# Optimization experiments

Hardware: AMD Instinct MI355X
Metric: run time of the kernel (lower is better)

The kernel has to match this reference:

```python
import jax, jax.numpy as jnp
import numpy as np

N, E, IN, H, C, L = 40000, 640000, 256, 128, 64, 4
ALPHA, LAMB = 0.5, 1.0


def setup_inputs() -> dict:
    key = jax.random.key(0)
    ks = jax.random.split(key, 8)
    x = jax.random.normal(ks[0], (N, IN), jnp.float32)
    src = jax.random.randint(ks[1], (E,), 0, N, jnp.int32)
    dst = jax.random.randint(ks[2], (E,), 0, N, jnp.int32)
    s_in = 1.0 / np.sqrt(IN)
    s_h = 1.0 / np.sqrt(H)
    fc1_w = jax.random.normal(ks[3], (IN, H), jnp.float32) * s_in
    fc1_b = jnp.zeros((H,), jnp.float32)
    W1 = jax.random.normal(ks[4], (L, H, H), jnp.float32) * s_h   # GCN2Conv weight1 per layer
    W2 = jax.random.normal(ks[5], (L, H, H), jnp.float32) * s_h   # GCN2Conv weight2 (initial-residual proj)
    bgc = jnp.zeros((L, H), jnp.float32)                          # GCN2Conv bias per layer
    fc2_w = jax.random.normal(ks[6], (H, C), jnp.float32) * s_h
    fc2_b = jnp.zeros((C,), jnp.float32)
    return dict(x=x, fc1_w=fc1_w, fc1_b=fc1_b, W1=W1, W2=W2, bgc=bgc,
                fc2_w=fc2_w, fc2_b=fc2_b, src=src, dst=dst)


def reference(x, fc1_w, fc1_b, W1, W2, bgc, fc2_w, fc2_b, src, dst):
    ones = jnp.ones((E,), x.dtype)
    # symmetric 'both' normalization: deg_out^{-1/2} on src side, deg_in^{-1/2} on dst side
    deg_out = jnp.clip(jax.ops.segment_sum(ones, src, num_segments=N), 1.0)
    deg_in = jnp.clip(jax.ops.segment_sum(ones, dst, num_segments=N), 1.0)
    norm_s = (deg_out ** -0.5)[:, None]
    norm_d = (deg_in ** -0.5)[:, None]

    # feature_preprocess: dropout (eval = identity) -> fc1 -> relu
    h0 = jax.nn.relu(x @ fc1_w + fc1_b)          # [N, H]
    h = h0
    for l in range(L):
        beta = float(np.log(LAMB / (l + 1) + 1.0))
        identity = h
        # sparse neighbor aggregation (SpMM via gather + segment_sum)
        agg = jax.ops.segment_sum((h * norm_s)[src], dst, num_segments=N) * norm_d
        feat = (1.0 - ALPHA) * agg               # smoothed features
        f0 = ALPHA * h0                          # initial residual
        rst = (1.0 - beta) * (feat + f0) + beta * (feat @ W1[l] + f0 @ W2[l]) + bgc[l]
        h = jax.nn.relu(rst + identity)          # outer residual + activation (dropout eval = identity)
    return h @ fc2_w + fc2_b                     # [N, C]
```

## Files before the change

### kernel.cpp

```cpp
#include <hip/hip_runtime.h>
#include <math.h>

#define N_NODES 40000
#define N_EDGES 640000
#define IN_F 256
#define H_F 128
#define C_F 64
#define L_LAYERS 4
#define SCAN_BLKS 157
#define N_CHUNKS 64
#define CHUNK_E 10000
#define HIST_WORDS 10000

typedef short short8 __attribute__((ext_vector_type(8)));
typedef unsigned short ushort8 __attribute__((ext_vector_type(8)));
typedef float f32x4 __attribute__((ext_vector_type(4)));

__device__ inline short to_bf16(float f) {
    unsigned u = __builtin_bit_cast(unsigned, f);
    unsigned r = (u + 0x7FFFu + ((u >> 16) & 1u)) >> 16;
    return (short)r;
}
__device__ inline float bf16_to_f(unsigned short u) {
    unsigned v = ((unsigned)u) << 16;
    return __builtin_bit_cast(float, v);
}

__device__ inline int block_excl_scan(int v, int* wsum, int* tot) {
    int tid = threadIdx.x;
    int lane = tid & 63, wid = tid >> 6;
    int incl = v;
    #pragma unroll
    for (int off = 1; off < 64; off <<= 1) {
        int t = __shfl_up(incl, off, 64);
        if (lane >= off) incl += t;
    }
    if (lane == 63) wsum[wid] = incl;
    __syncthreads();
    int prefix = 0, total = 0;
    #pragma unroll
    for (int w = 0; w < 4; w++) {
        int s = wsum[w];
        if (w < wid) prefix += s;
        total += s;
    }
    *tot = total;
    return prefix + incl - v;
}

#define CVT8(dstv, p) {                                                         \
    float4 _v0 = *(const float4*)(p); float4 _v1 = *(const float4*)((p) + 4);   \
    dstv[0] = to_bf16(_v0.x); dstv[1] = to_bf16(_v0.y);                         \
    dstv[2] = to_bf16(_v0.z); dstv[3] = to_bf16(_v0.w);                         \
    dstv[4] = to_bf16(_v1.x); dstv[5] = to_bf16(_v1.y);                         \
    dstv[6] = to_bf16(_v1.z); dstv[7] = to_bf16(_v1.w); }

__global__ __launch_bounds__(256) void prep_hist(const int* __restrict__ src,
                                                 const int* __restrict__ dst,
                                                 int* __restrict__ chunk_dst,
                                                 int* __restrict__ chunk_src,
                                                 unsigned char* __restrict__ lrank8,
                                                 const float* __restrict__ fc1_w,
                                                 const float* __restrict__ W1,
                                                 const float* __restrict__ W2,
                                                 const float* __restrict__ fc2_w,
                                                 float s0, float s1, float s2, float s3,
                                                 short* __restrict__ fc1_wT,
                                                 short* __restrict__ WcatT,
                                                 short* __restrict__ fc2_wT) {
    __shared__ int cntp[HIST_WORDS];
    int blk = blockIdx.x;
    if (blk < 128) {
        int role_dst = (blk < 64);
        int w = role_dst ? blk : blk - 64;
        const int* idx = role_dst ? dst : src;
        int base = w * CHUNK_E;
        for (int i = threadIdx.x; i < HIST_WORDS; i += 256) cntp[i] = 0;
        __syncthreads();
        if (role_dst) {
            for (int i = threadIdx.x; i < CHUNK_E; i += 256) {
                int d = idx[base + i];
                int sh = (d & 3) * 8;
                int old = atomicAdd(&cntp[d >> 2], 1 << sh);
                lrank8[base + i] = (unsigned char)((old >> sh) & 0xff);
            }
        } else {
            for (int i = threadIdx.x; i < CHUNK_E; i += 256) {
                int s = idx[base + i];
                atomicAdd(&cntp[s >> 2], 1 << ((s & 3) * 8));
            }
        }
        __syncthreads();
        int* outp = role_dst ? (chunk_dst + w * HIST_WORDS) : (chunk_src + w * HIST_WORDS);
        for (int i = threadIdx.x; i < HIST_WORDS; i += 256) outp[i] = cntp[i];
        return;
    }
    int i = (blk - 128) * 256 + threadIdx.x;
    if (i < 128 * 256) {
        int n = i >> 8, k = i & 255;
        fc1_wT[i] = to_bf16(fc1_w[k * H_F + n]);
    }
    if (i < 4 * 128 * 256) {
        int l = i >> 15; int r = i & 32767; int n = r >> 8; int k = r & 255;
        float sc = (l == 0) ? s0 : (l == 1) ? s1 : (l == 2) ? s2 : s3;
        float w = (k < 128) ? W1[l * 16384 + k * H_F + n]
                            : W2[l * 16384 + (k - 128) * H_F + n];
        WcatT[i] = to_bf16(sc * w);
    }
    if (i < 64 * 128) {
        int n = i >> 7, k = i & 127;
        fc2_wT[i] = to_bf16(fc2_w[k * C_F + n]);
    }
}

__global__ __launch_bounds__(256) void fc1_scan(const float* __restrict__ x,
                                                const short* __restrict__ wT,
                                                const float* __restrict__ b,
                                                unsigned short* __restrict__ h0b,
                                                const int* __restrict__ chunk_dst,
                                                const int* __restrict__ chunk_src,
                                                int* __restrict__ base32,
                                                float* __restrict__ rsq_in,
                                                float* __restrict__ rsq_out,
                                                float* __restrict__ sq_out,
                                                int* __restrict__ row_local,
                                                int* __restrict__ blk_sum) {
    __shared__ int wsum[4];
    int blk = blockIdx.x;
    if (blk >= 1250) {
        int sb = blk - 1250;
        int n = sb * 256 + threadIdx.x;
        int deg = 0, word = 0, sh = 0;
        if (n < N_NODES) {
            word = n >> 2; sh = (n & 3) * 8;
            #pragma unroll 4
            for (int w = 0; w < N_CHUNKS; w++)
                deg += (chunk_dst[w * HIST_WORDS + word] >> sh) & 0xff;
        }
        int tot;
        int excl = block_excl_scan(deg, wsum, &tot);
        if (n < N_NODES) {
            row_local[n] = excl;
            int run = excl;
            #pragma unroll 4
            for (int w = 0; w < N_CHUNKS; w++) {
                int v = (chunk_dst[w * HIST_WORDS + word] >> sh) & 0xff;
                base32[(size_t)w * N_NODES + n] = run;
                run += v;
            }
            int so = 0;
            #pragma unroll 4
            for (int w = 0; w < N_CHUNKS; w++)
                so += (chunk_src[w * HIST_WORDS + word] >> sh) & 0xff;
            float fd = (float)(deg < 1 ? 1 : deg);
            float fs = (float)(so < 1 ? 1 : so);
            rsq_in[n] = 1.0f / sqrtf(fd);
            rsq_out[n] = 1.0f / sqrtf(fs);
            sq_out[n] = sqrtf(fs);
        }
        if (threadIdx.x == 0) blk_sum[sb] = tot;
        return;
    }
    int tid = threadIdx.x;
    int wave = tid >> 6, lane = tid & 63;
    int rowgrp = wave >> 1, chalf = wave & 1;
    int m = lane & 15, quad = lane >> 4;
    int row = blk * 32 + rowgrp * 16 + m;
    const float* xr = x + (size_t)row * IN_F + quad * 8;
    short8 afrag[8];
    #pragma unroll
    for (int ks = 0; ks < 8; ks++) {
        CVT8(afrag[ks], xr + ks * 32);
    }
    #pragma unroll
    for (int ci = 0; ci < 4; ci += 2) {
        int c = chalf * 4 + ci;
        f32x4 acc0 = {0.f, 0.f, 0.f, 0.f};
        f32x4 acc1 = {0.f, 0.f, 0.f, 0.f};
        const short* b0p = wT + (size_t)(c * 16 + m) * IN_F + quad * 8;
        const short* b1p = b0p + 16 * IN_F;
        #pragma unroll
        for (int ks = 0; ks < 8; ks++) {
            short8 b0 = *(const short8*)(b0p + ks * 32);
            short8 b1 = *(const short8*)(b1p + ks * 32);
            acc0 = __builtin_amdgcn_mfma_f32_16x16x32_bf16(afrag[ks], b0, acc0, 0, 0, 0);
            acc1 = __builtin_amdgcn_mfma_f32_16x16x32_bf16(afrag[ks], b1, acc1, 0, 0, 0);
        }
        int col0 = c * 16 + m;
        int rbase = blk * 32 + rowgrp * 16 + quad * 4;
        float bg0 = b[col0], bg1 = b[col0 + 16];
        #pragma unroll
        for (int r = 0; r < 4; r++) {
            size_t idx2 = (size_t)(rbase + r) * H_F + col0;
            float v0 = acc0[r] + bg0;
            float v1 = acc1[r] + bg1;
            v0 = v0 > 0.f ? v0 : 0.f;
            v1 = v1 > 0.f ? v1 : 0.f;
            h0b[idx2] = (unsigned short)to_bf16(v0);
            h0b[idx2 + 16] = (unsigned short)to_bf16(v1);
        }
    }
}

__global__ __launch_bounds__(256) void fill_fused(const int* __restrict__ src,
                                                  const int* __restrict__ dst,
                                                  const unsigned char* __restrict__ lrank8,
                                                  const int* __restrict__ base32,
                                                  const int* __restrict__ row_local,
                                                  const int* __restrict__ blk_sum,
                                                  unsigned short* __restrict__ col16,
                                                  int* __restrict__ row_ptr,
                                                  const unsigned short* __restrict__ h0b,
                                                  const float* __restrict__ rsq_out,
                                                  unsigned short* __restrict__ h0s) {
    __shared__ int wsum[4];
    __shared__ int blk_offL[SCAN_BLKS];
    int tid = threadIdx.x;
    {
        int v = (tid < SCAN_BLKS) ? blk_sum[tid] : 0;
        int tot;
        int excl = block_excl_scan(v, wsum, &tot);
        if (tid < SCAN_BLKS) blk_offL[tid] = excl;
    }
    __syncthreads();

    int blk = blockIdx.x;
    if (blk < 2500) {
        int e = blk * 256 + tid;
        int w = e / CHUNK_E;
        int s = src[e], d = dst[e];
        int rp = blk_offL[d >> 8] + base32[(size_t)w * N_NODES + d] + (int)lrank8[e];
        col16[rp] = (unsigned short)s;
        return;
    }
    if (blk < 2657) {
        int n = (blk - 2500) * 256 + tid;
        if (n < N_NODES) row_ptr[n] = blk_offL[n >> 8] + row_local[n];
        if (blk == 2500 && tid == 0) row_ptr[N_NODES] = N_EDGES;
        return;
    }
    int j = (blk - 2657) * 2048 + tid * 8;
    ushort8 u = *(const ushort8*)(h0b + j);
    float rs = rsq_out[j >> 7];
    ushort8 o;
    #pragma unroll
    for (int jj = 0; jj < 8; jj++) o[jj] = (unsigned short)to_bf16(rs * bf16_to_f(u[jj]));
    *(ushort8*)(h0s + j) = o;
}

__global__ __launch_bounds__(256) void spmm_kernel(const unsigned short* __restrict__ hs,
                                                   const int* __restrict__ row_ptr,
                                                   const unsigned short* __restrict__ col16,
                                                   const float* __restrict__ rsq_in,
                                                   unsigned short* __restrict__ aggb) {
    int wave = threadIdx.x >> 6, lane = threadIdx.x & 63;
    int slot = lane >> 4, fi = lane & 15;
    int n = blockIdx.x * 4 + wave;
    int e0 = row_ptr[n], e1 = row_ptr[n + 1];
    float a[8] = {};
    for (int e = e0 + slot; e < e1; e += 16) {
        int eb = e + 4, ec = e + 8, ed = e + 12;
        int c0 = col16[e];
        int c1 = (eb < e1) ? col16[eb] : c0;  float w1 = (eb < e1) ? 1.f : 0.f;
        int c2 = (ec < e1) ? col16[ec] : c0;  float w2 = (ec < e1) ? 1.f : 0.f;
        int c3 = (ed < e1) ? col16[ed] : c0;  float w3 = (ed < e1) ? 1.f : 0.f;
        ushort8 u0 = *(const ushort8*)(hs + (size_t)c0 * H_F + fi * 8);
        ushort8 u1 = *(const ushort8*)(hs + (size_t)c1 * H_F + fi * 8);
        ushort8 u2 = *(const ushort8*)(hs + (size_t)c2 * H_F + fi * 8);
        ushort8 u3 = *(const ushort8*)(hs + (size_t)c3 * H_F + fi * 8);
        #pragma unroll
        for (int j = 0; j < 8; j++) {
            a[j] += bf16_to_f(u0[j]) + w1 * bf16_to_f(u1[j])
                  + w2 * bf16_to_f(u2[j]) + w3 * bf16_to_f(u3[j]);
        }
    }
    #pragma unroll
    for (int mask = 16; mask <= 32; mask <<= 1) {
        #pragma unroll
        for (int j = 0; j < 8; j++) a[j] += __shfl_xor(a[j], mask, 64);
    }
    if (slot == 0) {
        float rs = rsq_in[n];
        ushort8 r;
        #pragma unroll
        for (int j = 0; j < 8; j++) r[j] = (unsigned short)to_bf16(rs * a[j]);
        *(ushort8*)(aggb + (size_t)n * H_F + fi * 8) = r;
    }
}

__global__ __launch_bounds__(256) void combine_mfma(const unsigned short* __restrict__ aggb,
                                                    const unsigned short* __restrict__ h0b,
                                                    const unsigned short* __restrict__ hs_in,
                                                    const short* __restrict__ wT,
                                                    const float* __restrict__ bgc,
                                                    const float* __restrict__ rsq_out,
                                                    const float* __restrict__ sq_out,
                                                    float omb5,
                                                    unsigned short* __restrict__ hs_out) {
    int tid = threadIdx.x;
    int wave = tid >> 6, lane = tid & 63;
    int rowgrp = wave >> 1, chalf = wave & 1;
    int m = lane & 15, quad = lane >> 4;
    int row = blockIdx.x * 32 + rowgrp * 16 + m;
    const unsigned short* aggr = aggb + (size_t)row * H_F + quad * 8;
    const unsigned short* h0r  = h0b + (size_t)row * H_F + quad * 8;
    short8 afrag[8];
    #pragma unroll
    for (int ks = 0; ks < 4; ks++) {
        afrag[ks] = __builtin_bit_cast(short8, *(const ushort8*)(aggr + ks * 32));
        afrag[ks + 4] = __builtin_bit_cast(short8, *(const ushort8*)(h0r + ks * 32));
    }
    #pragma unroll
    for (int ci = 0; ci < 4; ci += 2) {
        int c = chalf * 4 + ci;
        f32x4 acc0 = {0.f, 0.f, 0.f, 0.f};
        f32x4 acc1 = {0.f, 0.f, 0.f, 0.f};
        const short* b0p = wT + (size_t)(c * 16 + m) * 256 + quad * 8;
        const short* b1p = b0p + 16 * 256;
        #pragma unroll
        for (int ks = 0; ks < 8; ks++) {
            short8 b0 = *(const short8*)(b0p + ks * 32);
            short8 b1 = *(const short8*)(b1p + ks * 32);
            acc0 = __builtin_amdgcn_mfma_f32_16x16x32_bf16(afrag[ks], b0, acc0, 0, 0, 0);
            acc1 = __builtin_amdgcn_mfma_f32_16x16x32_bf16(afrag[ks], b1, acc1, 0, 0, 0);
        }
        int col0 = c * 16 + m;
        int rbase = blockIdx.x * 32 + rowgrp * 16 + quad * 4;
        float bg0 = bgc[col0], bg1 = bgc[col0 + 16];
        #pragma unroll
        for (int r = 0; r < 4; r++) {
            int rw = rbase + r;
            size_t idx = (size_t)rw * H_F + col0;
            float sq = sq_out[rw];
            float rsq = rsq_out[rw];
            float s0 = bf16_to_f(aggb[idx]) + bf16_to_f(h0b[idx]);
            float s1 = bf16_to_f(aggb[idx + 16]) + bf16_to_f(h0b[idx + 16]);
            float v0 = omb5 * s0 + acc0[r] + bg0 + sq * bf16_to_f(hs_in[idx]);
            float v1 = omb5 * s1 + acc1[r] + bg1 + sq * bf16_to_f(hs_in[idx + 16]);
            v0 = v0 > 0.f ? v0 : 0.f;
            v1 = v1 > 0.f ? v1 : 0.f;
            hs_out[idx] = (unsigned short)to_bf16(rsq * v0);
            hs_out[idx + 16] = (unsigned short)to_bf16(rsq * v1);
        }
    }
}

__global__ __launch_bounds__(256) void fc2_mfma(const unsigned short* __restrict__ hs,
                                                const float* __restrict__ sq_out,
                                                const short* __restrict__ wT,
                                                const float* __restrict__ b,
                                                float* __restrict__ out) {
    int tid = threadIdx.x;
    int wave = tid >> 6, lane = tid & 63;
    int m = lane & 15, quad = lane >> 4;
    int row = blockIdx.x * 64 + wave * 16 + m;
    const unsigned short* hr = hs + (size_t)row * H_F + quad * 8;
    float sq = sq_out[row];
    short8 afrag[4];
    #pragma unroll
    for (int ks = 0; ks < 4; ks++) {
        ushort8 u = *(const ushort8*)(hr + ks * 32);
        #pragma unroll
        for (int j = 0; j < 8; j++) afrag[ks][j] = to_bf16(sq * bf16_to_f(u[j]));
    }
    #pragma unroll
    for (int c = 0; c < 4; c += 2) {
        f32x4 acc0 = {0.f, 0.f, 0.f, 0.f};
        f32x4 acc1 = {0.f, 0.f, 0.f, 0.f};
        const short* b0p = wT + (size_t)(c * 16 + m) * H_F + quad * 8;
        const short* b1p = b0p + 16 * H_F;
        #pragma unroll
        for (int ks = 0; ks < 4; ks++) {
            short8 b0 = *(const short8*)(b0p + ks * 32);
            short8 b1 = *(const short8*)(b1p + ks * 32);
            acc0 = __builtin_amdgcn_mfma_f32_16x16x32_bf16(afrag[ks], b0, acc0, 0, 0, 0);
            acc1 = __builtin_amdgcn_mfma_f32_16x16x32_bf16(afrag[ks], b1, acc1, 0, 0, 0);
        }
        int col0 = c * 16 + m;
        int rbase = blockIdx.x * 64 + wave * 16 + quad * 4;
        float bg0 = b[col0], bg1 = b[col0 + 16];
        #pragma unroll
        for (int r = 0; r < 4; r++) {
            size_t idx = (size_t)(rbase + r) * C_F + col0;
            out[idx] = acc0[r] + bg0;
            out[idx + 16] = acc1[r] + bg1;
        }
    }
}

extern "C" void kernel_launch(void* const* d_in, const int* in_sizes, int n_in,
                              void* d_out, int out_size, void* d_ws, size_t ws_size,
                              hipStream_t stream) {
    const float* x     = (const float*)d_in[0];
    const float* fc1_w = (const float*)d_in[1];
    const float* fc1_b = (const float*)d_in[2];
    const float* W1    = (const float*)d_in[3];
    const float* W2    = (const float*)d_in[4];
    const float* bgc   = (const float*)d_in[5];
    const float* fc2_w = (const float*)d_in[6];
    const float* fc2_b = (const float*)d_in[7];
    const int*   src   = (const int*)d_in[8];
    const int*   dst   = (const int*)d_in[9];
    float* out = (float*)d_out;

    char* p = (char*)d_ws;
    auto alloc = [&](size_t bytes) {
        char* r = p;
        p += (bytes + 255) & ~(size_t)255;
        return r;
    };
    int*   chunk_dst = (int*)alloc((size_t)N_CHUNKS * HIST_WORDS * 4);
    int*   chunk_src = (int*)alloc((size_t)N_CHUNKS * HIST_WORDS * 4);
    int*   base32    = (int*)alloc((size_t)N_CHUNKS * N_NODES * 4);
    unsigned char* lrank8 = (unsigned char*)alloc((size_t)N_EDGES);
    float* rsq_in  = (float*)alloc((size_t)N_NODES * 4);
    float* rsq_out = (float*)alloc((size_t)N_NODES * 4);
    float* sq_out  = (float*)alloc((size_t)N_NODES * 4);
    int*   row_ptr   = (int*)alloc((size_t)(N_NODES + 1) * 4);
    int*   row_local = (int*)alloc((size_t)N_NODES * 4);
    int*   blk_sum   = (int*)alloc((size_t)SCAN_BLKS * 4);
    unsigned short* col16 = (unsigned short*)alloc((size_t)N_EDGES * 2);
    unsigned short* aggb = (unsigned short*)alloc((size_t)N_NODES * H_F * 2);
    unsigned short* h0b  = (unsigned short*)alloc((size_t)N_NODES * H_F * 2);
    unsigned short* h0s  = (unsigned short*)alloc((size_t)N_NODES * H_F * 2);
    unsigned short* hAs  = (unsigned short*)alloc((size_t)N_NODES * H_F * 2);
    unsigned short* hBs  = (unsigned short*)alloc((size_t)N_NODES * H_F * 2);
    short* fc1_wT  = (short*)alloc((size_t)128 * 256 * 2);
    short* WcatT   = (short*)alloc((size_t)4 * 128 * 256 * 2);
    short* fc2_wT  = (short*)alloc((size_t)64 * 128 * 2);

    float beta[4], wscale[4], omb5[4];
    for (int l = 0; l < 4; l++) {
        beta[l] = (float)log(1.0 / (double)(l + 1) + 1.0);
        wscale[l] = 0.5f * beta[l];
        omb5[l] = 0.5f * (1.f - beta[l]);
    }

    prep_hist<<<640, 256, 0, stream>>>(src, dst, chunk_dst, chunk_src, lrank8,
                                       fc1_w, W1, W2, fc2_w,
                                       wscale[0], wscale[1], wscale[2], wscale[3],
                                       fc1_wT, WcatT, fc2_wT);
    fc1_scan<<<1407, 256, 0, stream>>>(x, fc1_wT, fc1_b, h0b,
                                       chunk_dst, chunk_src, base32,
                                       rsq_in, rsq_out, sq_out, row_local, blk_sum);
    fill_fused<<<5157, 256, 0, stream>>>(src, dst, lrank8, base32, row_local, blk_sum,
                                         col16, row_ptr, h0b, rsq_out, h0s);

    const unsigned short* sp_in[4] = {h0s, hAs, hBs, hAs};
    unsigned short* out_b[4]       = {hAs, hBs, hAs, hBs};
    for (int l = 0; l < L_LAYERS; l++) {
        spmm_kernel<<<N_NODES / 4, 256, 0, stream>>>(sp_in[l], row_ptr, col16,
                                                     rsq_in, aggb);
        combine_mfma<<<N_NODES / 32, 256, 0, stream>>>(aggb, h0b, sp_in[l],
                                                       WcatT + (size_t)l * 128 * 256,
                                                       bgc + (size_t)l * H_F,
                                                       rsq_out, sq_out, omb5[l],
                                                       out_b[l]);
    }
    fc2_mfma<<<N_NODES / 64, 256, 0, stream>>>(hBs, sq_out, fc2_wT, fc2_b, out);
}
```

Measured before the change: 370.7 us.

## Store scaled node features in feature-chunked layout for cache-local SpMM gathers

```diff
diff --git a/kernel.cpp b/kernel.cpp
--- a/kernel.cpp
+++ b/kernel.cpp
@@ -11,6 +11,8 @@
 #define N_CHUNKS 64
 #define CHUNK_E 10000
 #define HIST_WORDS 10000
+#define FCH 4
+#define FCW 32
 
 typedef short short8 __attribute__((ext_vector_type(8)));
 typedef unsigned short ushort8 __attribute__((ext_vector_type(8)));
@@ -127,8 +129,8 @@
                                                 int* __restrict__ blk_sum) {
     __shared__ int wsum[4];
     int blk = blockIdx.x;
-    if (blk >= 1250) {
-        int sb = blk - 1250;
+    if (blk >= 625) {
+        int sb = blk - 625;
         int n = sb * 256 + threadIdx.x;
         int deg = 0, word = 0, sh = 0;
         if (n < N_NODES) {
@@ -163,9 +165,8 @@
     }
     int tid = threadIdx.x;
     int wave = tid >> 6, lane = tid & 63;
-    int rowgrp = wave >> 1, chalf = wave & 1;
     int m = lane & 15, quad = lane >> 4;
-    int row = blk * 32 + rowgrp * 16 + m;
+    int row = blk * 64 + wave * 16 + m;
     const float* xr = x + (size_t)row * IN_F + quad * 8;
     short8 afrag[8];
     #pragma unroll
@@ -173,8 +174,7 @@
         CVT8(afrag[ks], xr + ks * 32);
     }
     #pragma unroll
-    for (int ci = 0; ci < 4; ci += 2) {
-        int c = chalf * 4 + ci;
+    for (int c = 0; c < 8; c += 2) {
         f32x4 acc0 = {0.f, 0.f, 0.f, 0.f};
         f32x4 acc1 = {0.f, 0.f, 0.f, 0.f};
         const short* b0p = wT + (size_t)(c * 16 + m) * IN_F + quad * 8;
@@ -187,7 +187,7 @@
             acc1 = __builtin_amdgcn_mfma_f32_16x16x32_bf16(afrag[ks], b1, acc1, 0, 0, 0);
         }
         int col0 = c * 16 + m;
-        int rbase = blk * 32 + rowgrp * 16 + quad * 4;
+        int rbase = blk * 64 + wave * 16 + quad * 4;
         float bg0 = b[col0], bg1 = b[col0 + 16];
         #pragma unroll
         for (int r = 0; r < 4; r++) {
@@ -212,7 +212,7 @@
                                                   int* __restrict__ row_ptr,
                                                   const unsigned short* __restrict__ h0b,
                                                   const float* __restrict__ rsq_out,
-                                                  unsigned short* __restrict__ h0s) {
+                                                  unsigned short* __restrict__ h0sC) {
     __shared__ int wsum[4];
     __shared__ int blk_offL[SCAN_BLKS];
     int tid = threadIdx.x;
@@ -240,42 +240,37 @@
         return;
     }
     int j = (blk - 2657) * 2048 + tid * 8;
+    int node = j >> 7, f = j & 127;
     ushort8 u = *(const ushort8*)(h0b + j);
-    float rs = rsq_out[j >> 7];
+    float rs = rsq_out[node];
     ushort8 o;
     #pragma unroll
     for (int jj = 0; jj < 8; jj++) o[jj] = (unsigned short)to_bf16(rs * bf16_to_f(u[jj]));
-    *(ushort8*)(h0s + j) = o;
-}
-
-__global__ __launch_bounds__(256) void spmm_kernel(const unsigned short* __restrict__ hs,
+    *(ushort8*)(h0sC + (size_t)(f >> 5) * N_NODES * FCW + node * FCW + (f & 31)) = o;
+}
+
+__global__ __launch_bounds__(256) void spmm_kernel(const unsigned short* __restrict__ hsC,
                                                    const int* __restrict__ row_ptr,
                                                    const unsigned short* __restrict__ col16,
                                                    const float* __restrict__ rsq_in,
                                                    unsigned short* __restrict__ aggb) {
     int wave = threadIdx.x >> 6, lane = threadIdx.x & 63;
-    int slot = lane >> 4, fi = lane & 15;
-    int n = blockIdx.x * 4 + wave;
+    int slot = lane >> 2, fi2 = lane & 3;
+    int blk = blockIdx.x;
+    int chunk = blk / 10000;
+    int nb = blk - chunk * 10000;
+    int n = nb * 4 + wave;
+    const unsigned short* hsrc = hsC + (size_t)chunk * N_NODES * FCW;
     int e0 = row_ptr[n], e1 = row_ptr[n + 1];
     float a[8] = {};
     for (int e = e0 + slot; e < e1; e += 16) {
-        int eb = e + 4, ec = e + 8, ed = e + 12;
-        int c0 = col16[e];
-        int c1 = (eb < e1) ? col16[eb] : c0;  float w1 = (eb < e1) ? 1.f : 0.f;
-        int c2 = (ec < e1) ? col16[ec] : c0;  float w2 = (ec < e1) ? 1.f : 0.f;
-        int c3 = (ed < e1) ? col16[ed] : c0;  float w3 = (ed < e1) ? 1.f : 0.f;
-        ushort8 u0 = *(const ushort8*)(hs + (size_t)c0 * H_F + fi * 8);
-        ushort8 u1 = *(const ushort8*)(hs + (size_t)c1 * H_F + fi * 8);
-        ushort8 u2 = *(const ushort8*)(hs + (size_t)c2 * H_F + fi * 8);
-        ushort8 u3 = *(const ushort8*)(hs + (size_t)c3 * H_F + fi * 8);
-        #pragma unroll
-        for (int j = 0; j < 8; j++) {
-            a[j] += bf16_to_f(u0[j]) + w1 * bf16_to_f(u1[j])
-                  + w2 * bf16_to_f(u2[j]) + w3 * bf16_to_f(u3[j]);
-        }
-    }
-    #pragma unroll
-    for (int mask = 16; mask <= 32; mask <<= 1) {
+        int c = col16[e];
+        ushort8 u = *(const ushort8*)(hsrc + (size_t)c * FCW + fi2 * 8);
+        #pragma unroll
+        for (int j = 0; j < 8; j++) a[j] += bf16_to_f(u[j]);
+    }
+    #pragma unroll
+    for (int mask = 4; mask <= 32; mask <<= 1) {
         #pragma unroll
         for (int j = 0; j < 8; j++) a[j] += __shfl_xor(a[j], mask, 64);
     }
@@ -284,7 +279,7 @@
         ushort8 r;
         #pragma unroll
         for (int j = 0; j < 8; j++) r[j] = (unsigned short)to_bf16(rs * a[j]);
-        *(ushort8*)(aggb + (size_t)n * H_F + fi * 8) = r;
+        *(ushort8*)(aggb + (size_t)n * H_F + chunk * FCW + fi2 * 8) = r;
     }
 }
 
@@ -325,27 +320,29 @@
             acc1 = __builtin_amdgcn_mfma_f32_16x16x32_bf16(afrag[ks], b1, acc1, 0, 0, 0);
         }
         int col0 = c * 16 + m;
+        size_t cb = (size_t)(c >> 1) * N_NODES * FCW;
         int rbase = blockIdx.x * 32 + rowgrp * 16 + quad * 4;
         float bg0 = bgc[col0], bg1 = bgc[col0 + 16];
         #pragma unroll
         for (int r = 0; r < 4; r++) {
             int rw = rbase + r;
             size_t idx = (size_t)rw * H_F + col0;
+            size_t cidx = cb + (size_t)rw * FCW + m;
             float sq = sq_out[rw];
             float rsq = rsq_out[rw];
             float s0 = bf16_to_f(aggb[idx]) + bf16_to_f(h0b[idx]);
             float s1 = bf16_to_f(aggb[idx + 16]) + bf16_to_f(h0b[idx + 16]);
-            float v0 = omb5 * s0 + acc0[r] + bg0 + sq * bf16_to_f(hs_in[idx]);
-            float v1 = omb5 * s1 + acc1[r] + bg1 + sq * bf16_to_f(hs_in[idx + 16]);
+            float v0 = omb5 * s0 + acc0[r] + bg0 + sq * bf16_to_f(hs_in[cidx]);
+            float v1 = omb5 * s1 + acc1[r] + bg1 + sq * bf16_to_f(hs_in[cidx + 16]);
             v0 = v0 > 0.f ? v0 : 0.f;
             v1 = v1 > 0.f ? v1 : 0.f;
-            hs_out[idx] = (unsigned short)to_bf16(rsq * v0);
-            hs_out[idx + 16] = (unsigned short)to_bf16(rsq * v1);
-        }
-    }
-}
-
-__global__ __launch_bounds__(256) void fc2_mfma(const unsigned short* __restrict__ hs,
+            hs_out[cidx] = (unsigned short)to_bf16(rsq * v0);
+            hs_out[cidx + 16] = (unsigned short)to_bf16(rsq * v1);
+        }
+    }
+}
+
+__global__ __launch_bounds__(256) void fc2_mfma(const unsigned short* __restrict__ hsC,
                                                 const float* __restrict__ sq_out,
                                                 const short* __restrict__ wT,
                                                 const float* __restrict__ b,
@@ -354,12 +351,12 @@
     int wave = tid >> 6, lane = tid & 63;
     int m = lane & 15, quad = lane >> 4;
     int row = blockIdx.x * 64 + wave * 16 + m;
-    const unsigned short* hr = hs + (size_t)row * H_F + quad * 8;
     float sq = sq_out[row];
     short8 afrag[4];
     #pragma unroll
     for (int ks = 0; ks < 4; ks++) {
-        ushort8 u = *(const ushort8*)(hr + ks * 32);
+        ushort8 u = *(const ushort8*)(hsC + (size_t)ks * N_NODES * FCW
+                                      + (size_t)row * FCW + quad * 8);
         #pragma unroll
         for (int j = 0; j < 8; j++) afrag[ks][j] = to_bf16(sq * bf16_to_f(u[j]));
     }
@@ -420,11 +417,11 @@
     int*   row_local = (int*)alloc((size_t)N_NODES * 4);
     int*   blk_sum   = (int*)alloc((size_t)SCAN_BLKS * 4);
     unsigned short* col16 = (unsigned short*)alloc((size_t)N_EDGES * 2);
-    unsigned short* aggb = (unsigned short*)alloc((size_t)N_NODES * H_F * 2);
-    unsigned short* h0b  = (unsigned short*)alloc((size_t)N_NODES * H_F * 2);
-    unsigned short* h0s  = (unsigned short*)alloc((size_t)N_NODES * H_F * 2);
-    unsigned short* hAs  = (unsigned short*)alloc((size_t)N_NODES * H_F * 2);
-    unsigned short* hBs  = (unsigned short*)alloc((size_t)N_NODES * H_F * 2);
+    unsigned short* aggb  = (unsigned short*)alloc((size_t)N_NODES * H_F * 2);
+    unsigned short* h0b   = (unsigned short*)alloc((size_t)N_NODES * H_F * 2);
+    unsigned short* h0sC  = (unsigned short*)alloc((size_t)N_NODES * H_F * 2);
+    unsigned short* hAsC  = (unsigned short*)alloc((size_t)N_NODES * H_F * 2);
+    unsigned short* hBsC  = (unsigned short*)alloc((size_t)N_NODES * H_F * 2);
     short* fc1_wT  = (short*)alloc((size_t)128 * 256 * 2);
     short* WcatT   = (short*)alloc((size_t)4 * 128 * 256 * 2);
     short* fc2_wT  = (short*)alloc((size_t)64 * 128 * 2);
@@ -440,16 +437,16 @@
                                        fc1_w, W1, W2, fc2_w,
                                        wscale[0], wscale[1], wscale[2], wscale[3],
                                        fc1_wT, WcatT, fc2_wT);
-    fc1_scan<<<1407, 256, 0, stream>>>(x, fc1_wT, fc1_b, h0b,
-                                       chunk_dst, chunk_src, base32,
-                                       rsq_in, rsq_out, sq_out, row_local, blk_sum);
+    fc1_scan<<<782, 256, 0, stream>>>(x, fc1_wT, fc1_b, h0b,
+                                      chunk_dst, chunk_src, base32,
+                                      rsq_in, rsq_out, sq_out, row_local, blk_sum);
     fill_fused<<<5157, 256, 0, stream>>>(src, dst, lrank8, base32, row_local, blk_sum,
-                                         col16, row_ptr, h0b, rsq_out, h0s);
-
-    const unsigned short* sp_in[4] = {h0s, hAs, hBs, hAs};
-    unsigned short* out_b[4]       = {hAs, hBs, hAs, hBs};
+                                         col16, row_ptr, h0b, rsq_out, h0sC);
+
+    const unsigned short* sp_in[4] = {h0sC, hAsC, hBsC, hAsC};
+    unsigned short* out_b[4]       = {hAsC, hBsC, hAsC, hBsC};
     for (int l = 0; l < L_LAYERS; l++) {
-        spmm_kernel<<<N_NODES / 4, 256, 0, stream>>>(sp_in[l], row_ptr, col16,
+        spmm_kernel<<<FCH * 10000, 256, 0, stream>>>(sp_in[l], row_ptr, col16,
                                                      rsq_in, aggb);
         combine_mfma<<<N_NODES / 32, 256, 0, stream>>>(aggb, h0b, sp_in[l],
                                                        WcatT + (size_t)l * 128 * 256,
@@ -457,5 +454,5 @@
                                                        rsq_out, sq_out, omb5[l],
                                                        out_b[l]);
     }
-    fc2_mfma<<<N_NODES / 64, 256, 0, stream>>>(hBs, sq_out, fc2_wT, fc2_b, out);
-}
+    fc2_mfma<<<N_NODES / 64, 256, 0, stream>>>(hBsC, sq_out, fc2_wT, fc2_b, out);
+}
```

New measurement: 499.3 us. 34.7% more time.
